# Optimization experiments

Measured on AMD Instinct MI355X. Metric: run time of the kernel, lower is better.

The kernel has to match this reference:

```python
import jax, jax.numpy as jnp
import numpy as np

N = 100000
IN_C = 256
HID = 128


def setup_inputs() -> dict:
    key = jax.random.key(0)
    ks = jax.random.split(key, 8)
    x = jax.random.normal(ks[0], (N, IN_C), dtype=jnp.float32)
    edge_index = jax.random.randint(ks[1], (2, 1600000), 0, N, dtype=jnp.int64)
    # GCNConv: lin (bias=False) + separate additive bias
    W1 = jax.random.normal(ks[2], (IN_C, HID), dtype=jnp.float32) / np.sqrt(IN_C)
    b1 = jnp.zeros((HID,), dtype=jnp.float32)
    W2 = jax.random.normal(ks[3], (HID, HID // 2), dtype=jnp.float32) / np.sqrt(HID)
    b2 = jnp.zeros((HID // 2,), dtype=jnp.float32)
    Wfc = jax.random.normal(ks[4], (HID // 2, 2), dtype=jnp.float32) / np.sqrt(HID // 2)
    bfc = jnp.zeros((2,), dtype=jnp.float32)
    return {"x": x, "edge_index": edge_index, "W1": W1, "b1": b1,
            "W2": W2, "b2": b2, "Wfc": Wfc, "bfc": bfc}


def _gcn_norm(edge_index, n):
    # add self-loops, symmetric normalization (PyG gcn_norm defaults)
    loop = jnp.arange(n, dtype=edge_index.dtype)
    src = jnp.concatenate([edge_index[0], loop])
    dst = jnp.concatenate([edge_index[1], loop])
    deg = jax.ops.segment_sum(jnp.ones_like(src, dtype=jnp.float32), dst,
                              num_segments=n)
    dinv = jnp.where(deg > 0, jax.lax.rsqrt(deg), 0.0)
    norm = dinv[src] * dinv[dst]  # [E + N]
    return src, dst, norm


def _gcn_conv(x, W, b, src, dst, norm, n):
    h = x @ W                       # [N, out] dense transform first
    msg = h[src] * norm[:, None]    # irregular gather, [E+N, out]
    out = jax.ops.segment_sum(msg, dst, num_segments=n)  # scatter-add
    return out + b


def reference(x, edge_index, W1, b1, W2, b2, Wfc, bfc):
    n = x.shape[0]
    src, dst, norm = _gcn_norm(edge_index, n)
    h = jax.nn.relu(_gcn_conv(x, W1, b1, src, dst, norm, n))
    # dropout is identity in eval mode
    h = jax.nn.relu(_gcn_conv(h, W2, b2, src, dst, norm, n))
    logits = h @ Wfc + bfc  # [N, 2]
    return jax.nn.log_softmax(logits, axis=1)
```

## Files before the change

kernel.cpp:

```cpp
#include <hip/hip_runtime.h>
#include <math.h>

#define IN_C 256
#define HID 128
#define H2  64
#define CAP 64

typedef __attribute__((ext_vector_type(8))) short bf16x8;
typedef __attribute__((ext_vector_type(4))) float f32x4;

__device__ __forceinline__ unsigned short f2bf(float f) {
  union { float f; unsigned int u; } v; v.f = f;
  unsigned int r = v.u + 0x7FFFu + ((v.u >> 16) & 1u);
  return (unsigned short)(r >> 16);
}
__device__ __forceinline__ float bf_lo(unsigned int u) {
  union { unsigned int u; float f; } v; v.u = u << 16; return v.f;
}
__device__ __forceinline__ float bf_hi(unsigned int u) {
  union { unsigned int u; float f; } v; v.u = u & 0xffff0000u; return v.f;
}
__device__ __forceinline__ unsigned int pack_bf(float lo, float hi) {
  return (unsigned int)f2bf(lo) | ((unsigned int)f2bf(hi) << 16);
}
__device__ __forceinline__ void add8w(float* a, uint4 u, float w) {
  a[0] += w * bf_lo(u.x); a[1] += w * bf_hi(u.x);
  a[2] += w * bf_lo(u.y); a[3] += w * bf_hi(u.y);
  a[4] += w * bf_lo(u.z); a[5] += w * bf_hi(u.z);
  a[6] += w * bf_lo(u.w); a[7] += w * bf_hi(u.w);
}
__device__ __forceinline__ void add8(float* a, uint4 u) {
  a[0] += bf_lo(u.x); a[1] += bf_hi(u.x);
  a[2] += bf_lo(u.y); a[3] += bf_hi(u.y);
  a[4] += bf_lo(u.z); a[5] += bf_hi(u.z);
  a[6] += bf_lo(u.w); a[7] += bf_hi(u.w);
}

__global__ void wcast_kernel(const float* __restrict__ W, unsigned short* __restrict__ Wt,
                             int K, int N) {
  int idx = blockIdx.x * 256 + threadIdx.x;
  if (idx < K * N) {
    int nn = idx / K, kk = idx % K;
    Wt[idx] = f2bf(W[kk * N + nn]);
  }
}

template <int K, int N, int BM, int WM, int WN, bool A_BF16>
__device__ __forceinline__ void gemm_body(const void* __restrict__ Av,
                                          const unsigned short* __restrict__ Bt,
                                          unsigned short* __restrict__ C, int M,
                                          int bidx, short* As, short* Bs) {
  constexpr int WTM = BM / WM;
  constexpr int WTN = N / WN;
  constexpr int MB = WTM / 16, NB = WTN / 16;
  constexpr int ACH = BM * 4 / 256;
  constexpr int BCH = N * 4 / 256;

  int tid = threadIdx.x;
  int lane = tid & 63, wid = tid >> 6;
  int ln15 = lane & 15, kg = lane >> 4;
  int wm = wid / WN, wn = wid % WN;
  int row0 = bidx * BM;

  f32x4 acc[MB][NB];
#pragma unroll
  for (int i = 0; i < MB; ++i)
#pragma unroll
    for (int j = 0; j < NB; ++j) acc[i][j] = (f32x4)0.0f;

  for (int k0 = 0; k0 < K; k0 += 32) {
#pragma unroll
    for (int p = 0; p < ACH; ++p) {
      int c = p * 256 + tid;
      int row = c >> 2, kc = c & 3;
      int grow = row0 + row;
      if (A_BF16) {
        const unsigned short* Ab = (const unsigned short*)Av;
        uint4 v = make_uint4(0, 0, 0, 0);
        if (grow < M) v = *reinterpret_cast<const uint4*>(&Ab[(size_t)grow * K + k0 + kc * 8]);
        *reinterpret_cast<uint4*>(&As[row * 40 + kc * 8]) = v;
      } else {
        const float* A = (const float*)Av;
        float4 v0 = make_float4(0.f, 0.f, 0.f, 0.f), v1 = v0;
        if (grow < M) {
          const float4* ap = reinterpret_cast<const float4*>(&A[(size_t)grow * K + k0 + kc * 8]);
          v0 = ap[0]; v1 = ap[1];
        }
        bf16x8 w;
        w[0] = (short)f2bf(v0.x); w[1] = (short)f2bf(v0.y);
        w[2] = (short)f2bf(v0.z); w[3] = (short)f2bf(v0.w);
        w[4] = (short)f2bf(v1.x); w[5] = (short)f2bf(v1.y);
        w[6] = (short)f2bf(v1.z); w[7] = (short)f2bf(v1.w);
        *reinterpret_cast<bf16x8*>(&As[row * 40 + kc * 8]) = w;
      }
    }
#pragma unroll
    for (int p = 0; p < BCH; ++p) {
      int c = p * 256 + tid;
      int nrow = c >> 2, kc = c & 3;
      *reinterpret_cast<uint4*>(&Bs[nrow * 40 + kc * 8]) =
          *reinterpret_cast<const uint4*>(&Bt[(size_t)nrow * K + k0 + kc * 8]);
    }
    __syncthreads();
    bf16x8 af[MB], bfr[NB];
#pragma unroll
    for (int mb = 0; mb < MB; ++mb)
      af[mb] = *reinterpret_cast<const bf16x8*>(&As[(wm * WTM + mb * 16 + ln15) * 40 + kg * 8]);
#pragma unroll
    for (int nb = 0; nb < NB; ++nb)
      bfr[nb] = *reinterpret_cast<const bf16x8*>(&Bs[(wn * WTN + nb * 16 + ln15) * 40 + kg * 8]);
#pragma unroll
    for (int mb = 0; mb < MB; ++mb)
#pragma unroll
      for (int nb = 0; nb < NB; ++nb)
        acc[mb][nb] = __builtin_amdgcn_mfma_f32_16x16x32_bf16(af[mb], bfr[nb], acc[mb][nb], 0, 0, 0);
    __syncthreads();
  }
#pragma unroll
  for (int mb = 0; mb < MB; ++mb)
#pragma unroll
    for (int nb = 0; nb < NB; ++nb) {
      int gcol = wn * WTN + nb * 16 + ln15;
#pragma unroll
      for (int q = 0; q < 4; ++q) {
        int grow = row0 + wm * WTM + mb * 16 + kg * 4 + q;
        if (grow < M) C[(size_t)grow * N + gcol] = f2bf(acc[mb][nb][q]);
      }
    }
}

__global__ __launch_bounds__(256) void fused_g1_place(
    const float* __restrict__ x, const unsigned short* __restrict__ W1T,
    unsigned short* __restrict__ h1lin, int M,
    const int* __restrict__ src, const int* __restrict__ dst, int E,
    int* __restrict__ fill, int* __restrict__ col, int GB, int PB) {
  __shared__ short smem[(64 + HID) * 40];
  int bid = blockIdx.x;
  int gp = GB < PB ? GB : PB;
  int m2 = 2 * gp;
  bool isPlace; int idx;
  if (bid < m2) { isPlace = (bid & 1); idx = bid >> 1; }
  else          { isPlace = (PB > GB); idx = gp + (bid - m2); }

  if (!isPlace) {
    gemm_body<IN_C, HID, 64, 2, 2, false>(x, W1T, h1lin, M, idx, smem, smem + 64 * 40);
  } else {
    int tid = threadIdx.x;
    int base = idx * 1024;
    int dd[4], ss[4], sl[4]; bool ok[4];
#pragma unroll
    for (int j = 0; j < 4; ++j) {
      int e = base + j * 256 + tid;
      ok[j] = e < E;
      dd[j] = ok[j] ? dst[e] : 0;
      ss[j] = ok[j] ? src[e] : 0;
    }
#pragma unroll
    for (int j = 0; j < 4; ++j)
      sl[j] = ok[j] ? atomicAdd(&fill[dd[j]], 1) : CAP;
#pragma unroll
    for (int j = 0; j < 4; ++j)
      if (ok[j] && sl[j] < CAP) col[(size_t)dd[j] * CAP + sl[j]] = ss[j];
  }
}

__global__ __launch_bounds__(256) void gemm2_kernel(const unsigned short* __restrict__ A,
                                                    const unsigned short* __restrict__ Bt,
                                                    unsigned short* __restrict__ C, int M) {
  __shared__ short smem[(64 + H2) * 40];
  gemm_body<HID, H2, 64, 2, 2, true>(A, Bt, C, M, blockIdx.x, smem, smem + 64 * 40);
}

__global__ __launch_bounds__(256) void agg1_kernel(const uint4* __restrict__ hs4,
    const int* __restrict__ fill, const int* __restrict__ col,
    const float* __restrict__ bias, uint4* __restrict__ outb, int n) {
  int sub = threadIdx.x >> 4, l = threadIdx.x & 15;
  int i = blockIdx.x * 16 + sub;
  if (i >= n) return;
  int degi = fill[i];
  float di = rsqrtf((float)(degi + 1));
  int cnt = degi > CAP ? CAP : degi;
  const int* cp = col + (size_t)i * CAP;
  float a[8];
  uint4 us = hs4[(size_t)i * 16 + l];
  a[0] = di * bf_lo(us.x); a[1] = di * bf_hi(us.x);
  a[2] = di * bf_lo(us.y); a[3] = di * bf_hi(us.y);
  a[4] = di * bf_lo(us.z); a[5] = di * bf_hi(us.z);
  a[6] = di * bf_lo(us.w); a[7] = di * bf_hi(us.w);
  int k = 0;
  for (; k + 7 < cnt; k += 8) {
    int c[8], f[8]; uint4 u[8];
#pragma unroll
    for (int j = 0; j < 8; ++j) c[j] = cp[k + j];
#pragma unroll
    for (int j = 0; j < 8; ++j) { f[j] = fill[c[j]]; u[j] = hs4[(size_t)c[j] * 16 + l]; }
#pragma unroll
    for (int j = 0; j < 8; ++j) add8w(a, u[j], rsqrtf((float)(f[j] + 1)));
  }
  for (; k + 3 < cnt; k += 4) {
    int c[4], f[4]; uint4 u[4];
#pragma unroll
    for (int j = 0; j < 4; ++j) c[j] = cp[k + j];
#pragma unroll
    for (int j = 0; j < 4; ++j) { f[j] = fill[c[j]]; u[j] = hs4[(size_t)c[j] * 16 + l]; }
#pragma unroll
    for (int j = 0; j < 4; ++j) add8w(a, u[j], rsqrtf((float)(f[j] + 1)));
  }
  for (; k < cnt; ++k) {
    int c = cp[k];
    float w = rsqrtf((float)(fill[c] + 1));
    add8w(a, hs4[(size_t)c * 16 + l], w);
  }
  float4 bA = reinterpret_cast<const float4*>(bias)[2 * l];
  float4 bB = reinterpret_cast<const float4*>(bias)[2 * l + 1];
  float r0 = di * fmaxf(di * a[0] + bA.x, 0.f);
  float r1 = di * fmaxf(di * a[1] + bA.y, 0.f);
  float r2 = di * fmaxf(di * a[2] + bA.z, 0.f);
  float r3 = di * fmaxf(di * a[3] + bA.w, 0.f);
  float r4 = di * fmaxf(di * a[4] + bB.x, 0.f);
  float r5 = di * fmaxf(di * a[5] + bB.y, 0.f);
  float r6 = di * fmaxf(di * a[6] + bB.z, 0.f);
  float r7 = di * fmaxf(di * a[7] + bB.w, 0.f);
  uint4 o;
  o.x = pack_bf(r0, r1); o.y = pack_bf(r2, r3);
  o.z = pack_bf(r4, r5); o.w = pack_bf(r6, r7);
  outb[(size_t)i * 16 + l] = o;
}

__global__ __launch_bounds__(256) void agg2fc_kernel(const uint4* __restrict__ hs4,
    const int* __restrict__ fill, const int* __restrict__ col,
    const float* __restrict__ bias, const float* __restrict__ Wfc,
    const float* __restrict__ bfc, float* __restrict__ out, int n) {
  int sub = threadIdx.x >> 3, l = threadIdx.x & 7;
  int i = blockIdx.x * 32 + sub;
  if (i >= n) return;
  int degi = fill[i];
  float di = rsqrtf((float)(degi + 1));
  int cnt = degi > CAP ? CAP : degi;
  const int* cp = col + (size_t)i * CAP;
  float a[8];
  uint4 us = hs4[(size_t)i * 8 + l];
  a[0] = bf_lo(us.x); a[1] = bf_hi(us.x);
  a[2] = bf_lo(us.y); a[3] = bf_hi(us.y);
  a[4] = bf_lo(us.z); a[5] = bf_hi(us.z);
  a[6] = bf_lo(us.w); a[7] = bf_hi(us.w);
  int k = 0;
  for (; k + 7 < cnt; k += 8) {
    int c[8]; uint4 u[8];
#pragma unroll
    for (int j = 0; j < 8; ++j) c[j] = cp[k + j];
#pragma unroll
    for (int j = 0; j < 8; ++j) u[j] = hs4[(size_t)c[j] * 8 + l];
#pragma unroll
    for (int j = 0; j < 8; ++j) add8(a, u[j]);
  }
  for (; k + 3 < cnt; k += 4) {
    int c[4]; uint4 u[4];
#pragma unroll
    for (int j = 0; j < 4; ++j) c[j] = cp[k + j];
#pragma unroll
    for (int j = 0; j < 4; ++j) u[j] = hs4[(size_t)c[j] * 8 + l];
#pragma unroll
    for (int j = 0; j < 4; ++j) add8(a, u[j]);
  }
  for (; k < cnt; ++k) add8(a, hs4[(size_t)cp[k] * 8 + l]);
  float4 bA = reinterpret_cast<const float4*>(bias)[2 * l];
  float4 bB = reinterpret_cast<const float4*>(bias)[2 * l + 1];
  float r[8];
  r[0] = fmaxf(di * a[0] + bA.x, 0.f);
  r[1] = fmaxf(di * a[1] + bA.y, 0.f);
  r[2] = fmaxf(di * a[2] + bA.z, 0.f);
  r[3] = fmaxf(di * a[3] + bA.w, 0.f);
  r[4] = fmaxf(di * a[4] + bB.x, 0.f);
  r[5] = fmaxf(di * a[5] + bB.y, 0.f);
  r[6] = fmaxf(di * a[6] + bB.z, 0.f);
  r[7] = fmaxf(di * a[7] + bB.w, 0.f);
  float p0 = 0.f, p1 = 0.f;
#pragma unroll
  for (int s = 0; s < 4; ++s) {
    float4 w = reinterpret_cast<const float4*>(Wfc)[4 * l + s];
    p0 += r[2 * s] * w.x + r[2 * s + 1] * w.z;
    p1 += r[2 * s] * w.y + r[2 * s + 1] * w.w;
  }
#pragma unroll
  for (int off = 4; off; off >>= 1) {
    p0 += __shfl_xor(p0, off, 8);
    p1 += __shfl_xor(p1, off, 8);
  }
  if (l == 0) {
    float l0 = p0 + bfc[0], l1 = p1 + bfc[1];
    float m = fmaxf(l0, l1);
    float lse = m + logf(expf(l0 - m) + expf(l1 - m));
    float2 o; o.x = l0 - lse; o.y = l1 - lse;
    reinterpret_cast<float2*>(out)[i] = o;
  }
}

extern "C" void kernel_launch(void* const* d_in, const int* in_sizes, int n_in,
                              void* d_out, int out_size, void* d_ws, size_t ws_size,
                              hipStream_t stream) {
  const float* x   = (const float*)d_in[0];
  const int*   ei  = (const int*)d_in[1];
  const float* W1  = (const float*)d_in[2];
  const float* b1  = (const float*)d_in[3];
  const float* W2  = (const float*)d_in[4];
  const float* b2  = (const float*)d_in[5];
  const float* Wfc = (const float*)d_in[6];
  const float* bfc = (const float*)d_in[7];
  float* out = (float*)d_out;

  int n = in_sizes[0] / IN_C;
  int E = in_sizes[1] / 2;
  const int* src = ei;
  const int* dst = ei + E;

  char* ws = (char*)d_ws;
  size_t off = 0;
  auto alloc = [&](size_t bytes) {
    void* p = ws + off;
    off = (off + bytes + 255) & ~(size_t)255;
    return p;
  };
  int*   fill   = (int*)alloc((size_t)n * 4);
  int*   col    = (int*)alloc((size_t)n * CAP * 4);
  unsigned short* h1lin = (unsigned short*)alloc((size_t)n * HID * 2);
  unsigned short* h1    = (unsigned short*)alloc((size_t)n * HID * 2);
  unsigned short* h2lin = (unsigned short*)alloc((size_t)n * H2 * 2);
  unsigned short* W1T   = (unsigned short*)alloc((size_t)IN_C * HID * 2);
  unsigned short* W2T   = (unsigned short*)alloc((size_t)HID * H2 * 2);

  hipMemsetAsync(fill, 0, (size_t)n * 4, stream);
  wcast_kernel<<<(IN_C * HID + 255) / 256, 256, 0, stream>>>(W1, W1T, IN_C, HID);
  wcast_kernel<<<(HID * H2 + 255) / 256, 256, 0, stream>>>(W2, W2T, HID, H2);

  int GB = (n + 63) / 64;
  int PB = (E + 1023) / 1024;
  fused_g1_place<<<GB + PB, 256, 0, stream>>>(x, W1T, h1lin, n, src, dst, E, fill, col, GB, PB);

  agg1_kernel<<<(n + 15) / 16, 256, 0, stream>>>((const uint4*)h1lin, fill, col, b1, (uint4*)h1, n);
  gemm2_kernel<<<(n + 63) / 64, 256, 0, stream>>>(h1, W2T, h2lin, n);
  agg2fc_kernel<<<(n + 31) / 32, 256, 0, stream>>>((const uint4*)h2lin, fill, col, b2, Wfc, bfc, out, n);
}
```

Baseline: 199.5 us.

## Build adjacency via two-pass bucketed scatter instead of global atomics

Replaces the per-edge global atomicAdd placement (fused with GEMM1) with a two-pass build. Edges are first binned into 256-node buckets using shared-memory counters and one global atomic per bucket per block. A second kernel then builds the per-node column lists with LDS atomics. This is meant to cut global atomic contention and scattered writes, at the cost of an extra pass over a packed slab buffer, fixed NBK/BSLAB constants tied to N, and no longer overlapping GEMM1 with edge placement.

```diff
diff --git a/kernel.cpp b/kernel.cpp
--- a/kernel.cpp
+++ b/kernel.cpp
@@ -5,6 +5,8 @@
 #define HID 128
 #define H2  64
 #define CAP 64
+#define NBK 391
+#define BSLAB 8192
 
 typedef __attribute__((ext_vector_type(8))) short bf16x8;
 typedef __attribute__((ext_vector_type(4))) float f32x4;
@@ -43,6 +45,61 @@
     int nn = idx / K, kk = idx % K;
     Wt[idx] = f2bf(W[kk * N + nn]);
   }
+}
+
+__global__ __launch_bounds__(256) void scatter_kernel(
+    const int* __restrict__ src, const int* __restrict__ dstA, int E,
+    int* __restrict__ bucketFill , unsigned int* __restrict__ packed) {
+  __shared__ int cnt[NBK];
+  __shared__ int base[NBK];
+  int tid = threadIdx.x;
+  for (int i = tid; i < NBK; i += 256) cnt[i] = 0;
+  __syncthreads();
+  int e0 = blockIdx.x * 2048;
+  int bk[8], ls[8]; unsigned int sv[8]; bool ok[8];
+#pragma unroll
+  for (int j = 0; j < 8; ++j) {
+    int e = e0 + j * 256 + tid;
+    ok[j] = e < E;
+    int d = ok[j] ? dstA[e] : 0;
+    int s = ok[j] ? src[e] : 0;
+    bk[j] = d >> 8;
+    sv[j] = ((unsigned int)s << 8) | (unsigned int)(d & 255);
+    ls[j] = ok[j] ? atomicAdd(&cnt[bk[j]], 1) : 0;
+  }
+  __syncthreads();
+  for (int i = tid; i < NBK; i += 256)
+    base[i] = cnt[i] ? atomicAdd(&bucketFill[i * 16], cnt[i]) : 0;
+  __syncthreads();
+#pragma unroll
+  for (int j = 0; j < 8; ++j)
+    if (ok[j]) {
+      int pos = base[bk[j]] + ls[j];
+      if (pos < BSLAB) packed[(size_t)bk[j] * BSLAB + pos] = sv[j];
+    }
+}
+
+__global__ __launch_bounds__(256) void bucket_csr_kernel(
+    const unsigned int* __restrict__ packed, const int* __restrict__ bucketFill,
+    int* __restrict__ fill, int* __restrict__ col, int n) {
+  __shared__ int lcnt[256];
+  int b = blockIdx.x;
+  int t = threadIdx.x;
+  lcnt[t] = 0;
+  __syncthreads();
+  int m = bucketFill[b * 16];
+  if (m > BSLAB) m = BSLAB;
+  const unsigned int* pp = packed + (size_t)b * BSLAB;
+  int node0 = b * 256;
+  for (int i = t; i < m; i += 256) {
+    unsigned int p = pp[i];
+    int lo = p & 255;
+    int slot = atomicAdd(&lcnt[lo], 1);
+    if (slot < CAP) col[(size_t)(node0 + lo) * CAP + slot] = (int)(p >> 8);
+  }
+  __syncthreads();
+  int node = node0 + t;
+  if (node < n) fill[node] = lcnt[t];
 }
 
 template <int K, int N, int BM, int WM, int WN, bool A_BF16>
@@ -129,39 +186,11 @@
     }
 }
 
-__global__ __launch_bounds__(256) void fused_g1_place(
-    const float* __restrict__ x, const unsigned short* __restrict__ W1T,
-    unsigned short* __restrict__ h1lin, int M,
-    const int* __restrict__ src, const int* __restrict__ dst, int E,
-    int* __restrict__ fill, int* __restrict__ col, int GB, int PB) {
+__global__ __launch_bounds__(256) void gemm1_kernel(const float* __restrict__ A,
+                                                    const unsigned short* __restrict__ Bt,
+                                                    unsigned short* __restrict__ C, int M) {
   __shared__ short smem[(64 + HID) * 40];
-  int bid = blockIdx.x;
-  int gp = GB < PB ? GB : PB;
-  int m2 = 2 * gp;
-  bool isPlace; int idx;
-  if (bid < m2) { isPlace = (bid & 1); idx = bid >> 1; }
-  else          { isPlace = (PB > GB); idx = gp + (bid - m2); }
-
-  if (!isPlace) {
-    gemm_body<IN_C, HID, 64, 2, 2, false>(x, W1T, h1lin, M, idx, smem, smem + 64 * 40);
-  } else {
-    int tid = threadIdx.x;
-    int base = idx * 1024;
-    int dd[4], ss[4], sl[4]; bool ok[4];
-#pragma unroll
-    for (int j = 0; j < 4; ++j) {
-      int e = base + j * 256 + tid;
-      ok[j] = e < E;
-      dd[j] = ok[j] ? dst[e] : 0;
-      ss[j] = ok[j] ? src[e] : 0;
-    }
-#pragma unroll
-    for (int j = 0; j < 4; ++j)
-      sl[j] = ok[j] ? atomicAdd(&fill[dd[j]], 1) : CAP;
-#pragma unroll
-    for (int j = 0; j < 4; ++j)
-      if (ok[j] && sl[j] < CAP) col[(size_t)dd[j] * CAP + sl[j]] = ss[j];
-  }
+  gemm_body<IN_C, HID, 64, 2, 2, false>(A, Bt, C, M, blockIdx.x, smem, smem + 64 * 40);
 }
 
 __global__ __launch_bounds__(256) void gemm2_kernel(const unsigned short* __restrict__ A,
@@ -321,7 +350,9 @@
     off = (off + bytes + 255) & ~(size_t)255;
     return p;
   };
-  int*   fill   = (int*)alloc((size_t)n * 4);
+  int*   fill       = (int*)alloc((size_t)n * 4);
+  int*   bucketFill = (int*)alloc((size_t)NBK * 16 * 4);
+  unsigned int* packed = (unsigned int*)alloc((size_t)NBK * BSLAB * 4);
   int*   col    = (int*)alloc((size_t)n * CAP * 4);
   unsigned short* h1lin = (unsigned short*)alloc((size_t)n * HID * 2);
   unsigned short* h1    = (unsigned short*)alloc((size_t)n * HID * 2);
@@ -329,14 +360,14 @@
   unsigned short* W1T   = (unsigned short*)alloc((size_t)IN_C * HID * 2);
   unsigned short* W2T   = (unsigned short*)alloc((size_t)HID * H2 * 2);
 
-  hipMemsetAsync(fill, 0, (size_t)n * 4, stream);
+  hipMemsetAsync(bucketFill, 0, (size_t)NBK * 16 * 4, stream);
   wcast_kernel<<<(IN_C * HID + 255) / 256, 256, 0, stream>>>(W1, W1T, IN_C, HID);
   wcast_kernel<<<(HID * H2 + 255) / 256, 256, 0, stream>>>(W2, W2T, HID, H2);
 
-  int GB = (n + 63) / 64;
-  int PB = (E + 1023) / 1024;
-  fused_g1_place<<<GB + PB, 256, 0, stream>>>(x, W1T, h1lin, n, src, dst, E, fill, col, GB, PB);
-
+  scatter_kernel<<<(E + 2047) / 2048, 256, 0, stream>>>(src, dst, E, bucketFill, packed);
+  bucket_csr_kernel<<<NBK, 256, 0, stream>>>(packed, bucketFill, fill, col, n);
+
+  gemm1_kernel<<<(n + 63) / 64, 256, 0, stream>>>(x, W1T, h1lin, n);
   agg1_kernel<<<(n + 15) / 16, 256, 0, stream>>>((const uint4*)h1lin, fill, col, b1, (uint4*)h1, n);
   gemm2_kernel<<<(n + 63) / 64, 256, 0, stream>>>(h1, W2T, h2lin, n);
   agg2fc_kernel<<<(n + 31) / 32, 256, 0, stream>>>((const uint4*)h2lin, fill, col, b2, Wfc, bfc, out, n);
```

Result: no change. 197.9 us (-0.8%).
